# Performance work log

Hardware: AMD Instinct MI355X
Metric: run time of the kernel (lower is better)

Reference implementation:

```python
import jax, jax.numpy as jnp
import numpy as np

B, T, D = 512, 200, 512

def setup_inputs() -> dict:
    key = jax.random.key(0)
    k1, k2, k3 = jax.random.split(key, 3)
    inputs = jax.random.normal(k1, (B, T, D), dtype=jnp.float32)
    # Keras 'uniform' initializer -> U(-0.05, 0.05)
    W = jax.random.uniform(k2, (T, T), minval=-0.05, maxval=0.05, dtype=jnp.float32)
    b = jax.random.uniform(k3, (T,), minval=-0.05, maxval=0.05, dtype=jnp.float32)
    return {"inputs": inputs, "W": W, "b": b}

def reference(inputs, W, b):
    # x = permute(inputs, (0,2,1)) -> [B, D, T]; scores over timestep axis
    # a = softmax(tanh(x @ W + b)) along last axis (T)
    scores = jnp.tanh(jnp.einsum('btd,ts->bds', inputs, W) + b)  # [B, D, T]
    a = jax.nn.softmax(scores, axis=-1)                           # softmax over T
    # permute back to [B, T, D], elementwise multiply, sum over T -> [B, D]
    out = jnp.einsum('bdt,btd->bd', a, inputs)
    return out
```

## Files before the change

kernel.cpp:

```cpp
#include <hip/hip_runtime.h>
#include <cstdint>
#include <cstddef>

#define B_DIM 512
#define T_DIM 200
#define D_DIM 512
#define NPAD  208
#define NKG   28
#define NT    13
#define KS_STEPS 7
#define SLICE 3208

typedef short  short8  __attribute__((ext_vector_type(8)));
typedef float  floatx4 __attribute__((ext_vector_type(4)));

__device__ __forceinline__ unsigned short f2bf(float f) {
  unsigned int u = __float_as_uint(f);
  u += 0x7fffu + ((u >> 16) & 1u);
  return (unsigned short)(u >> 16);
}
__device__ __forceinline__ float bf2f(unsigned short h) {
  return __uint_as_float(((unsigned int)h) << 16);
}
__device__ __forceinline__ unsigned int cvt_pk_bf16(float a, float b) {
  unsigned int d;
  asm("v_cvt_pk_bf16_f32 %0, %1, %2" : "=v"(d) : "v"(a), "v"(b));
  return d;
}

__global__ void prep_w_kernel(const float* __restrict__ W,
                              unsigned short* __restrict__ wf) {
  int idx = blockIdx.x * blockDim.x + threadIdx.x;
  if (idx >= NKG * 8 * NPAD) return;
  int k = idx / NPAD;
  int n = idx - k * NPAD;
  float v = (k < T_DIM && n < T_DIM) ? W[k * T_DIM + n] : 0.0f;
  wf[((size_t)(k >> 3) * NPAD + n) * 8 + (k & 7)] = f2bf(v);
}

__global__ __launch_bounds__(256, 4)
void attn_kernel(const float* __restrict__ X,
                 const unsigned short* __restrict__ wf,
                 const float* __restrict__ bias,
                 float* __restrict__ out) {
  __shared__ __align__(16) unsigned short Xs[2 * SLICE];
  __shared__ __align__(16) float comb[4][32][2];

  const int tid  = threadIdx.x;
  const int wv   = tid >> 6;
  const int lane = tid & 63;
  const int l15  = lane & 15;
  const int g    = lane >> 4;

  const int bid  = blockIdx.x;
  const int bb   = bid >> 4;
  const int dblk = (bid & 15) << 5;

  {
    const float* xb = X + (size_t)bb * (T_DIM * D_DIM) + dblk;
    #pragma unroll
    for (int it = 0; it < 7; ++it) {
      int i = it * 256 + tid;
      if (it < 6 || tid < 64) {
        int t  = i >> 3;
        int c4 = i & 7;
        float4 v = *(const float4*)(xb + (size_t)t * D_DIM + (c4 << 2));
        unsigned short* dst = Xs + (c4 >> 2) * SLICE
                            + ((t >> 3) * 16 + ((c4 & 3) << 2)) * 8 + (t & 7);
        unsigned int w01 = cvt_pk_bf16(v.x, v.y);
        unsigned int w23 = cvt_pk_bf16(v.z, v.w);
        dst[0]  = (unsigned short)(w01 & 0xffffu);
        dst[8]  = (unsigned short)(w01 >> 16);
        dst[16] = (unsigned short)(w23 & 0xffffu);
        dst[24] = (unsigned short)(w23 >> 16);
      }
    }
  }
  __syncthreads();

  const int nt0 = (wv == 0) ? 0 : (1 + 3 * wv);
  const int ntw = (wv == 0) ? 4 : 3;

  floatx4 acc[2][4];
  #pragma unroll
  for (int h = 0; h < 2; ++h)
    #pragma unroll
    for (int j = 0; j < 4; ++j)
      acc[h][j] = (floatx4){0.f, 0.f, 0.f, 0.f};

  const unsigned short* wk = wf + ((size_t)g * NPAD + nt0 * 16 + l15) * 8;

  short8 bc[4], bn[4];
  short8 a0c, a1c, a0n, a1n;

  #pragma unroll
  for (int j = 0; j < 4; ++j)
    if (j < ntw) bc[j] = *(const short8*)(wk + j * 128);
  a0c = *(const short8*)&Xs[(g * 16 + l15) * 8];
  a1c = *(const short8*)&Xs[SLICE + (g * 16 + l15) * 8];

  #pragma unroll
  for (int ks = 0; ks < KS_STEPS; ++ks) {
    if (ks < 6) {
      const unsigned short* wkn = wk + (size_t)(ks + 1) * (4 * NPAD * 8);
      #pragma unroll
      for (int j = 0; j < 4; ++j)
        if (j < ntw) bn[j] = *(const short8*)(wkn + j * 128);
      const int kgn = (ks + 1) * 4 + g;
      if (ks < 5 || g == 0) {
        a0n = *(const short8*)&Xs[(kgn * 16 + l15) * 8];
        a1n = *(const short8*)&Xs[SLICE + (kgn * 16 + l15) * 8];
      } else {
        a0n = (short8){0, 0, 0, 0, 0, 0, 0, 0};
        a1n = (short8){0, 0, 0, 0, 0, 0, 0, 0};
      }
    }
    #pragma unroll
    for (int j = 0; j < 4; ++j)
      if (j < ntw) {
        acc[0][j] = __builtin_amdgcn_mfma_f32_16x16x32_bf16(a0c, bc[j], acc[0][j], 0, 0, 0);
        acc[1][j] = __builtin_amdgcn_mfma_f32_16x16x32_bf16(a1c, bc[j], acc[1][j], 0, 0, 0);
      }
    if (ks < 6) {
      a0c = a0n; a1c = a1n;
      #pragma unroll
      for (int j = 0; j < 4; ++j) bc[j] = bn[j];
    }
  }

  float part[2][4], rs[2][4];
  #pragma unroll
  for (int h = 0; h < 2; ++h)
    #pragma unroll
    for (int r = 0; r < 4; ++r) { part[h][r] = 0.f; rs[h][r] = 0.f; }

  #pragma unroll
  for (int j = 0; j < 4; ++j) {
    if (j < ntw) {
      const int nt = nt0 + j;
      const int t  = nt * 16 + l15;
      const bool valid = (t < T_DIM);
      const int tc = valid ? t : (T_DIM - 1);
      const float bvn = bias[tc];
      const unsigned short* xp = &Xs[((tc >> 3) * 16) * 8 + (tc & 7)];
      #pragma unroll
      for (int r = 0; r < 4; ++r) {
        const int m = g * 4 + r;
        #pragma unroll
        for (int h = 0; h < 2; ++h) {
          float z  = acc[h][j][r] + bvn;
          float e  = __expf(2.0f * z);
          float th = 1.0f - __fdividef(2.0f, e + 1.0f);
          float p  = valid ? __expf(th) : 0.0f;
          rs[h][r]   += p;
          part[h][r] += p * bf2f(xp[h * SLICE + m * 8]);
        }
      }
    }
  }
  #pragma unroll
  for (int off = 1; off <= 8; off <<= 1)
    #pragma unroll
    for (int h = 0; h < 2; ++h)
      #pragma unroll
      for (int r = 0; r < 4; ++r) {
        part[h][r] += __shfl_xor(part[h][r], off, 16);
        rs[h][r]   += __shfl_xor(rs[h][r],   off, 16);
      }

  if (l15 == 0) {
    #pragma unroll
    for (int h = 0; h < 2; ++h)
      #pragma unroll
      for (int r = 0; r < 4; ++r) {
        comb[wv][h * 16 + g * 4 + r][0] = part[h][r];
        comb[wv][h * 16 + g * 4 + r][1] = rs[h][r];
      }
  }
  __syncthreads();

  if (tid < 32) {
    float ps = 0.f, ss = 0.f;
    #pragma unroll
    for (int w = 0; w < 4; ++w) {
      ps += comb[w][tid][0];
      ss += comb[w][tid][1];
    }
    out[(size_t)bb * D_DIM + dblk + tid] = ps * __frcp_rn(ss);
  }
}

extern "C" void kernel_launch(void* const* d_in, const int* in_sizes, int n_in,
                              void* d_out, int out_size, void* d_ws, size_t ws_size,
                              hipStream_t stream) {
  const float* X  = (const float*)d_in[0];
  const float* W  = (const float*)d_in[1];
  const float* bs = (const float*)d_in[2];
  float* out = (float*)d_out;
  unsigned short* wf = (unsigned short*)d_ws;

  const int wtot = NKG * 8 * NPAD;
  hipLaunchKernelGGL(prep_w_kernel, dim3((wtot + 255) / 256), dim3(256), 0, stream,
                     W, wf);
  hipLaunchKernelGGL(attn_kernel, dim3(8192), dim3(256), 0, stream,
                     X, wf, bs, out);
}
```

Measured before the change: 319.6 us.

## Widen d-tile to 64 columns per block to reuse W fragments across four MFMA rows

Each block now handles 64 d-columns instead of 32, halving the grid and loading each W fragment once for four MFMA A-tiles instead of two. This cuts global/L2 traffic for the bf16 W matrix. The explicit software prefetch (double-buffered A/B registers) is removed in favour of straightforward per-step loads. The larger tile doubles LDS use and accumulator registers, which may lower occupancy under the launch bounds and expose load latency without the prefetch.

```diff
diff --git a/kernel.cpp b/kernel.cpp
--- a/kernel.cpp
+++ b/kernel.cpp
@@ -43,8 +43,8 @@
                  const unsigned short* __restrict__ wf,
                  const float* __restrict__ bias,
                  float* __restrict__ out) {
-  __shared__ __align__(16) unsigned short Xs[2 * SLICE];
-  __shared__ __align__(16) float comb[4][32][2];
+  __shared__ __align__(16) unsigned short Xs[4 * SLICE];
+  __shared__ __align__(16) float comb[4][64][2];
 
   const int tid  = threadIdx.x;
   const int wv   = tid >> 6;
@@ -53,17 +53,17 @@
   const int g    = lane >> 4;
 
   const int bid  = blockIdx.x;
-  const int bb   = bid >> 4;
-  const int dblk = (bid & 15) << 5;
+  const int bb   = bid >> 3;
+  const int dblk = (bid & 7) << 6;
 
   {
     const float* xb = X + (size_t)bb * (T_DIM * D_DIM) + dblk;
     #pragma unroll
-    for (int it = 0; it < 7; ++it) {
+    for (int it = 0; it < 13; ++it) {
       int i = it * 256 + tid;
-      if (it < 6 || tid < 64) {
-        int t  = i >> 3;
-        int c4 = i & 7;
+      if (it < 12 || tid < 128) {
+        int t  = i >> 4;
+        int c4 = i & 15;
         float4 v = *(const float4*)(xb + (size_t)t * D_DIM + (c4 << 2));
         unsigned short* dst = Xs + (c4 >> 2) * SLICE
                             + ((t >> 3) * 16 + ((c4 & 3) << 2)) * 8 + (t & 7);
@@ -81,56 +81,40 @@
   const int nt0 = (wv == 0) ? 0 : (1 + 3 * wv);
   const int ntw = (wv == 0) ? 4 : 3;
 
-  floatx4 acc[2][4];
+  floatx4 acc[4][4];
   #pragma unroll
-  for (int h = 0; h < 2; ++h)
+  for (int h = 0; h < 4; ++h)
     #pragma unroll
     for (int j = 0; j < 4; ++j)
       acc[h][j] = (floatx4){0.f, 0.f, 0.f, 0.f};
 
   const unsigned short* wk = wf + ((size_t)g * NPAD + nt0 * 16 + l15) * 8;
 
-  short8 bc[4], bn[4];
-  short8 a0c, a1c, a0n, a1n;
-
-  #pragma unroll
-  for (int j = 0; j < 4; ++j)
-    if (j < ntw) bc[j] = *(const short8*)(wk + j * 128);
-  a0c = *(const short8*)&Xs[(g * 16 + l15) * 8];
-  a1c = *(const short8*)&Xs[SLICE + (g * 16 + l15) * 8];
-
   #pragma unroll
   for (int ks = 0; ks < KS_STEPS; ++ks) {
-    if (ks < 6) {
-      const unsigned short* wkn = wk + (size_t)(ks + 1) * (4 * NPAD * 8);
-      #pragma unroll
-      for (int j = 0; j < 4; ++j)
-        if (j < ntw) bn[j] = *(const short8*)(wkn + j * 128);
-      const int kgn = (ks + 1) * 4 + g;
-      if (ks < 5 || g == 0) {
-        a0n = *(const short8*)&Xs[(kgn * 16 + l15) * 8];
-        a1n = *(const short8*)&Xs[SLICE + (kgn * 16 + l15) * 8];
-      } else {
-        a0n = (short8){0, 0, 0, 0, 0, 0, 0, 0};
-        a1n = (short8){0, 0, 0, 0, 0, 0, 0, 0};
-      }
-    }
+    const int kg = ks * 4 + g;
+    short8 b[4];
+    #pragma unroll
+    for (int j = 0; j < 4; ++j)
+      if (j < ntw) b[j] = *(const short8*)(wk + (size_t)ks * (4 * NPAD * 8) + j * 128);
+    const bool av = (ks < 6) || (g == 0);
+    short8 a[4];
+    #pragma unroll
+    for (int h = 0; h < 4; ++h)
+      a[h] = av ? *(const short8*)&Xs[h * SLICE + (kg * 16 + l15) * 8]
+                : (short8){0, 0, 0, 0, 0, 0, 0, 0};
     #pragma unroll
     for (int j = 0; j < 4; ++j)
       if (j < ntw) {
-        acc[0][j] = __builtin_amdgcn_mfma_f32_16x16x32_bf16(a0c, bc[j], acc[0][j], 0, 0, 0);
-        acc[1][j] = __builtin_amdgcn_mfma_f32_16x16x32_bf16(a1c, bc[j], acc[1][j], 0, 0, 0);
+        #pragma unroll
+        for (int h = 0; h < 4; ++h)
+          acc[h][j] = __builtin_amdgcn_mfma_f32_16x16x32_bf16(a[h], b[j], acc[h][j], 0, 0, 0);
       }
-    if (ks < 6) {
-      a0c = a0n; a1c = a1n;
-      #pragma unroll
-      for (int j = 0; j < 4; ++j) bc[j] = bn[j];
-    }
   }
 
-  float part[2][4], rs[2][4];
+  float part[4][4], rs[4][4];
   #pragma unroll
-  for (int h = 0; h < 2; ++h)
+  for (int h = 0; h < 4; ++h)
     #pragma unroll
     for (int r = 0; r < 4; ++r) { part[h][r] = 0.f; rs[h][r] = 0.f; }
 
@@ -147,7 +131,7 @@
       for (int r = 0; r < 4; ++r) {
         const int m = g * 4 + r;
         #pragma unroll
-        for (int h = 0; h < 2; ++h) {
+        for (int h = 0; h < 4; ++h) {
           float z  = acc[h][j][r] + bvn;
           float e  = __expf(2.0f * z);
           float th = 1.0f - __fdividef(2.0f, e + 1.0f);
@@ -161,7 +145,7 @@
   #pragma unroll
   for (int off = 1; off <= 8; off <<= 1)
     #pragma unroll
-    for (int h = 0; h < 2; ++h)
+    for (int h = 0; h < 4; ++h)
       #pragma unroll
       for (int r = 0; r < 4; ++r) {
         part[h][r] += __shfl_xor(part[h][r], off, 16);
@@ -170,7 +154,7 @@
 
   if (l15 == 0) {
     #pragma unroll
-    for (int h = 0; h < 2; ++h)
+    for (int h = 0; h < 4; ++h)
       #pragma unroll
       for (int r = 0; r < 4; ++r) {
         comb[wv][h * 16 + g * 4 + r][0] = part[h][r];
@@ -179,7 +163,7 @@
   }
   __syncthreads();
 
-  if (tid < 32) {
+  if (tid < 64) {
     float ps = 0.f, ss = 0.f;
     #pragma unroll
     for (int w = 0; w < 4; ++w) {
@@ -202,6 +186,6 @@
   const int wtot = NKG * 8 * NPAD;
   hipLaunchKernelGGL(prep_w_kernel, dim3((wtot + 255) / 256), dim3(256), 0, stream,
                      W, wf);
-  hipLaunchKernelGGL(attn_kernel, dim3(8192), dim3(256), 0, stream,
+  hipLaunchKernelGGL(attn_kernel, dim3(4096), dim3(256), 0, stream,
                      X, wf, bs, out);
 }
```

Result: no change. 317.7 us (-0.6%).
